# Kernel optimization log

Hardware: AMD Instinct MI355X
Metric: run time of the kernel (lower is better)

## Reference

```python
import jax, jax.numpy as jnp
import numpy as np

ALPHA = 300.0   # attractor_alpha
N_ATT = 16      # n_attractors
MIN_D = 0.001
MAX_D = 10.0


def _resize_bilinear_ac(x, out_h, out_w):
    """Bilinear resize with align_corners=True on trailing (H, W) dims of [B,C,h,w]."""
    h, w = x.shape[-2], x.shape[-1]
    ys = jnp.arange(out_h, dtype=jnp.float32) * ((h - 1) / max(out_h - 1, 1))
    xs = jnp.arange(out_w, dtype=jnp.float32) * ((w - 1) / max(out_w - 1, 1))
    y0 = jnp.floor(ys).astype(jnp.int32); y1 = jnp.minimum(y0 + 1, h - 1)
    x0 = jnp.floor(xs).astype(jnp.int32); x1 = jnp.minimum(x0 + 1, w - 1)
    wy = (ys - y0.astype(jnp.float32))[:, None]   # [out_h, 1]
    wx = (xs - x0.astype(jnp.float32))[None, :]   # [1, out_w]
    v00 = x[..., y0[:, None], x0[None, :]]
    v01 = x[..., y0[:, None], x1[None, :]]
    v10 = x[..., y1[:, None], x0[None, :]]
    v11 = x[..., y1[:, None], x1[None, :]]
    top = v00 * (1 - wx) + v01 * wx
    bot = v10 * (1 - wx) + v11 * wx
    return top * (1 - wy) + bot * wy


def setup_inputs() -> dict:
    key = jax.random.key(0)
    k = jax.random.split(key, 7)
    B, C, H, W = 4, 128, 192, 192
    n_bins = 64
    x = jax.random.normal(k[0], (B, C, H, W), dtype=jnp.float32)
    prev_bin = jax.random.uniform(k[1], (B, n_bins, H // 2, W // 2), dtype=jnp.float32)
    prev_bin_embedding = jax.random.normal(k[2], (B, C, H // 2, W // 2), dtype=jnp.float32)
    w1 = jax.random.normal(k[3], (128, 128), dtype=jnp.float32) * 0.05
    b1 = jnp.zeros((128,), dtype=jnp.float32)
    w2 = jax.random.normal(k[4], (2 * N_ATT, 128), dtype=jnp.float32) * 0.05
    b2 = jnp.zeros((2 * N_ATT,), dtype=jnp.float32)
    return {"x": x, "prev_bin": prev_bin, "prev_bin_embedding": prev_bin_embedding,
            "w1": w1, "b1": b1, "w2": w2, "b2": b2}


def reference(x, prev_bin, prev_bin_embedding, w1, b1, w2, b2):
    B, C, H, W = x.shape
    # add (interpolated) previous bin embedding
    pe = _resize_bilinear_ac(prev_bin_embedding, H, W)
    h = x + pe
    # per-pixel MLP (two 1x1 convs)
    h = jax.nn.relu(jnp.einsum('bchw,oc->bohw', h, w1) + b1[:, None, None])
    att = jax.nn.relu(jnp.einsum('bchw,oc->bohw', h, w2) + b2[:, None, None]) + 0.001
    # [B, n_attractors, 2, H, W] -> take normed attractor points
    att = att.reshape(B, N_ATT, 2, H, W)[:, :, 0]          # [B, nA, H, W]
    # upsample previous bin centers to feature resolution
    bc = _resize_bilinear_ac(prev_bin, H, W)               # [B, nB, H, W]
    # broadcast-subtract + inverse attractor + mean over attractors
    dx = att[:, :, None, :, :] - bc[:, None, :, :, :]      # [B, nA, nB, H, W]
    delta_c = jnp.mean(dx / (1.0 + ALPHA * dx * dx), axis=1)  # gamma = 2
    bin_new_centers = bc + delta_c
    bin_centers = (MAX_D - MIN_D) * bin_new_centers + MIN_D
    bin_centers = jnp.clip(jnp.sort(bin_centers, axis=1), MIN_D, MAX_D)
    return bin_new_centers, bin_centers
```

## Files before the change

kernel.cpp:

```cpp
#include <hip/hip_runtime.h>

constexpr int Bc = 4, Cc = 128, Hc = 192, Wc = 192;
constexpr int HI = 96, WI = 96;
constexpr int NB = 64;
constexpr int NA = 16;
constexpr float SCL = 95.0f / 191.0f;

typedef __attribute__((ext_vector_type(8))) short bf16x8;
typedef __attribute__((ext_vector_type(4))) float f32x4;

__device__ __forceinline__ unsigned short f2bf(float f) {
  unsigned u = __builtin_bit_cast(unsigned, f);
  unsigned r = (u + 0x7FFFu + ((u >> 16) & 1u)) >> 16;
  return (unsigned short)r;
}
__device__ __forceinline__ float rcp_fast(float r) {
#if defined(__has_builtin)
#if __has_builtin(__builtin_amdgcn_rcpf)
  return __builtin_amdgcn_rcpf(r);
#else
  return 1.0f / r;
#endif
#else
  return 1.0f / r;
#endif
}

__global__ __launch_bounds__(256) void k_prep(
    const float* __restrict__ w1, const float* __restrict__ w2,
    unsigned short* __restrict__ w1p, unsigned short* __restrict__ w2p)
{
  const int t = blockIdx.x * 256 + threadIdx.x;
  if (t < 16384) {
    const int e  = t & 7;
    const int l  = (t >> 3) & 63;
    const int kt = (t >> 9) & 3;
    const int nt = t >> 11;
    const int n  = nt * 16 + (l & 15);
    const int k  = kt * 32 + (l >> 4) * 8 + e;
    w1p[t] = f2bf(w1[n * 128 + k]);
  } else {
    const int u  = t - 16384;
    const int e  = u & 7;
    const int l  = (u >> 3) & 63;
    const int kt = u >> 9;
    const int n  = 2 * (l & 15);
    const int k  = kt * 32 + (l >> 4) * 8 + e;
    w2p[u] = f2bf(w2[n * 128 + k]);
  }
}

__global__ __launch_bounds__(256, 3) void k_att(
    const float* __restrict__ x, const float* __restrict__ pbe,
    const unsigned short* __restrict__ w1p, const float* __restrict__ b1,
    const unsigned short* __restrict__ w2p, const float* __restrict__ b2,
    float* __restrict__ att)
{
  constexpr int PH = 136;
  constexpr int RP = 37;
  __shared__ __align__(16) unsigned char smem[32768 + 128 * RP * 4];
  unsigned short* w1_s  = (unsigned short*)smem;
  float*          row_s = (float*)(smem + 32768);
  unsigned short* a1_s  = (unsigned short*)(smem + 32768);

  const int tid = threadIdx.x;
  const int xg0 = blockIdx.x * 64;
  const int y = blockIdx.y;
  const int b = blockIdx.z;

  const float ysf = y * SCL;
  const int y0 = (int)ysf;
  const int y1 = min(y0 + 1, HI - 1);
  const float wy = ysf - (float)y0;
  const int xi0 = (int)(xg0 * SCL);

  const int lane = tid & 63;
  const int wv = tid >> 6;
  const int ln = lane & 15;
  const int qd = lane >> 4;
  const int m0 = wv * 16;

  const int px = m0 + ln;
  const int xg = xg0 + px;
  const float xsf = (float)xg * SCL;
  const int x0i = (int)xsf;
  const float wx = xsf - (float)x0i;
  const int xl = x0i - xi0;

  float4 wstage[8];
  {
    const float4* wp4 = (const float4*)w1p;
    #pragma unroll
    for (int i = 0; i < 8; ++i) wstage[i] = wp4[tid + 256 * i];
  }

  bf16x8 b2f[4];
  #pragma unroll
  for (int kt = 0; kt < 4; ++kt)
    b2f[kt] = *(const bf16x8*)&w2p[kt * 512 + lane * 8];
  float bias1[8];
  #pragma unroll
  for (int nt = 0; nt < 8; ++nt) bias1[nt] = b1[nt * 16 + ln];
  const float bias2 = b2[2 * ln];

  float xr[32];
  #pragma unroll
  for (int kt = 0; kt < 4; ++kt) {
    #pragma unroll
    for (int j = 0; j < 8; ++j) {
      const int c = kt * 32 + qd * 8 + j;
      xr[kt * 8 + j] = x[((size_t)(b * Cc + c) * Hc + y) * Wc + xg];
    }
  }

  #pragma unroll
  for (int i = 0; i < 18; ++i) {
    const int f = tid + 256 * i;
    const int c = f / 36;
    const int xi = f - c * 36;
    const int xgl = min(xi0 + xi, WI - 1);
    const float* p = pbe + (size_t)(b * Cc + c) * (HI * WI);
    const float top = p[y0 * WI + xgl];
    const float bot = p[y1 * WI + xgl];
    row_s[c * RP + xi] = top + wy * (bot - top);
  }

  {
    float4* ws4 = (float4*)w1_s;
    #pragma unroll
    for (int i = 0; i < 8; ++i) ws4[tid + 256 * i] = wstage[i];
  }
  __syncthreads();

  bf16x8 af[4];
  #pragma unroll
  for (int kt = 0; kt < 4; ++kt) {
    #pragma unroll
    for (int j = 0; j < 8; ++j) {
      const int c = kt * 32 + qd * 8 + j;
      const float v0 = row_s[c * RP + xl];
      const float v1 = row_s[c * RP + xl + 1];
      af[kt][j] = (short)f2bf(xr[kt * 8 + j] + v0 + wx * (v1 - v0));
    }
  }
  __syncthreads();

  f32x4 acc[8];
  #pragma unroll
  for (int nt = 0; nt < 8; ++nt) acc[nt] = f32x4{0.f, 0.f, 0.f, 0.f};
  #pragma unroll
  for (int nt = 0; nt < 8; ++nt) {
    #pragma unroll
    for (int kt = 0; kt < 4; ++kt) {
      const bf16x8 bf = *(const bf16x8*)&w1_s[(nt * 4 + kt) * 512 + lane * 8];
      acc[nt] = __builtin_amdgcn_mfma_f32_16x16x32_bf16(af[kt], bf, acc[nt], 0, 0, 0);
    }
  }

  #pragma unroll
  for (int nt = 0; nt < 8; ++nt) {
    const int n = nt * 16 + ln;
    const float bias = bias1[nt];
    #pragma unroll
    for (int r = 0; r < 4; ++r) {
      const int m = m0 + qd * 4 + r;
      a1_s[m * PH + n] = f2bf(fmaxf(acc[nt][r] + bias, 0.f));
    }
  }

  f32x4 acc2 = f32x4{0.f, 0.f, 0.f, 0.f};
  #pragma unroll
  for (int kt = 0; kt < 4; ++kt) {
    const bf16x8 a2 = *(const bf16x8*)&a1_s[(m0 + ln) * PH + kt * 32 + qd * 8];
    acc2 = __builtin_amdgcn_mfma_f32_16x16x32_bf16(a2, b2f[kt], acc2, 0, 0, 0);
  }
  #pragma unroll
  for (int r = 0; r < 4; ++r) {
    const int opx = m0 + qd * 4 + r;
    const float v = fmaxf(acc2[r] + bias2, 0.f) + 0.001f;
    att[((size_t)((b * Hc + y) * Wc) + xg0 + opx) * NA + ln] = v;
  }
}

__global__ __launch_bounds__(192, 2) void k_bins(
    const float* __restrict__ pb, const float* __restrict__ att,
    float* __restrict__ out0, float* __restrict__ out1)
{
  __shared__ __align__(16) float row_s[NB][WI];

  const int tid = threadIdx.x;
  const int y = blockIdx.x;
  const int b = blockIdx.y;

  const float ysf = y * SCL;
  const int y0 = (int)ysf;
  const int y1 = min(y0 + 1, HI - 1);
  const float wy = ysf - (float)y0;

  float am[16];
  {
    const float4* ap = (const float4*)(att + ((size_t)((b * Hc + y) * Wc) + tid) * NA);
    const float4 a0 = ap[0], a1 = ap[1], a2 = ap[2], a3 = ap[3];
    am[0] = a0.x;  am[1] = a0.y;  am[2] = a0.z;  am[3] = a0.w;
    am[4] = a1.x;  am[5] = a1.y;  am[6] = a1.z;  am[7] = a1.w;
    am[8] = a2.x;  am[9] = a2.y;  am[10] = a2.z; am[11] = a2.w;
    am[12] = a3.x; am[13] = a3.y; am[14] = a3.z; am[15] = a3.w;
  }

  #pragma unroll
  for (int i = 0; i < 8; ++i) {
    const int u = tid + 192 * i;
    const int k = u / 24;
    const int g = u - k * 24;
    const float* base = pb + (size_t)(b * NB + k) * (HI * WI);
    const float4 t4 = *(const float4*)&base[y0 * WI + g * 4];
    const float4 b4 = *(const float4*)&base[y1 * WI + g * 4];
    float4 r;
    r.x = t4.x + wy * (b4.x - t4.x);
    r.y = t4.y + wy * (b4.y - t4.y);
    r.z = t4.z + wy * (b4.z - t4.z);
    r.w = t4.w + wy * (b4.w - t4.w);
    *(float4*)&row_s[k][g * 4] = r;
  }
  __syncthreads();

  const float xsf = tid * SCL;
  const int x0 = (int)xsf;
  const float wx = xsf - (float)x0;

  const size_t obase = (size_t)(b * NB) * (Hc * Wc) + (size_t)y * Wc + tid;
  float v[NB];

  #pragma unroll
  for (int kb = 0; kb < NB; kb += 4) {
    float bc[4], dl[4];
    #pragma unroll
    for (int q = 0; q < 4; ++q) {
      const int k = kb + q;
      const float v0 = row_s[k][x0], v1 = row_s[k][x0 + 1];
      bc[q] = v0 + wx * (v1 - v0);
      dl[q] = 0.f;
    }
    #pragma unroll
    for (int j = 0; j < NA; ++j) {
      const float a = am[j];
      #pragma unroll
      for (int q = 0; q < 4; ++q) {
        const float d = a - bc[q];
        const float rq = fmaf(300.f * d, d, 1.f);
        dl[q] = fmaf(d, rcp_fast(rq), dl[q]);
      }
    }
    #pragma unroll
    for (int q = 0; q < 4; ++q) {
      const float bnc = fmaf(dl[q], 1.f / 16.f, bc[q]);
      out0[obase + (size_t)(kb + q) * (Hc * Wc)] = bnc;
      v[kb + q] = fmaf(9.999f, bnc, 0.001f);
    }
  }

  #pragma unroll
  for (int size = 2; size <= NB; size <<= 1) {
    #pragma unroll
    for (int stride = size >> 1; stride >= 1; stride >>= 1) {
      #pragma unroll
      for (int i = 0; i < NB; ++i) {
        if ((i & stride) == 0) {
          const int j = i | stride;
          const bool asc = ((i & size) == 0);
          const float a = v[i], c = v[j];
          const float lo = fminf(a, c), hi = fmaxf(a, c);
          v[i] = asc ? lo : hi;
          v[j] = asc ? hi : lo;
        }
      }
    }
  }

  #pragma unroll
  for (int k = 0; k < NB; ++k) {
    out1[obase + (size_t)k * (Hc * Wc)] = fminf(fmaxf(v[k], 0.001f), 10.0f);
  }
}

extern "C" void kernel_launch(void* const* d_in, const int* in_sizes, int n_in,
                              void* d_out, int out_size, void* d_ws, size_t ws_size,
                              hipStream_t stream) {
  const float* x   = (const float*)d_in[0];
  const float* pb  = (const float*)d_in[1];
  const float* pbe = (const float*)d_in[2];
  const float* w1  = (const float*)d_in[3];
  const float* b1  = (const float*)d_in[4];
  const float* w2  = (const float*)d_in[5];
  const float* b2  = (const float*)d_in[6];

  float* out0 = (float*)d_out;
  float* out1 = out0 + (size_t)Bc * NB * Hc * Wc;

  unsigned short* w1p = (unsigned short*)d_ws;
  unsigned short* w2p = w1p + 16384;
  float* att = (float*)((char*)d_ws + 65536);

  k_prep<<<72, 256, 0, stream>>>(w1, w2, w1p, w2p);

  dim3 g1(Wc / 64, Hc, Bc);
  k_att<<<g1, 256, 0, stream>>>(x, pbe, w1p, b1, w2p, b2, att);

  dim3 g2(Hc, Bc);
  k_bins<<<g2, 192, 0, stream>>>(pb, att, out0, out1);
}
```

Baseline: 217.3 us.

## Split k_bins bins across two thread halves with shared-memory bitonic merge

Each pixel is now handled by two threads, each computing and sorting 32 of the 64 bins in opposite directions. The halves are then merged through shared memory with a compare-exchange step followed by a 32-element bitonic merge. This halves per-thread register use (v[32] instead of v[64]) and doubles block size so occupancy and parallelism rise. In exchange it adds extra syncthreads and shared-memory traffic, and each attractor load is duplicated across the two halves.

Result: faster. 213.0 us (-2.0%).

```diff
diff --git a/kernel.cpp b/kernel.cpp
--- a/kernel.cpp
+++ b/kernel.cpp
@@ -182,13 +182,16 @@
   }
 }
 
-__global__ __launch_bounds__(192, 2) void k_bins(
+__global__ __launch_bounds__(384, 4) void k_bins(
     const float* __restrict__ pb, const float* __restrict__ att,
     float* __restrict__ out0, float* __restrict__ out1)
 {
   __shared__ __align__(16) float row_s[NB][WI];
+  float* xch = &row_s[0][0];
 
   const int tid = threadIdx.x;
+  const int h = (tid >= 192) ? 1 : 0;
+  const int px = tid - 192 * h;
   const int y = blockIdx.x;
   const int b = blockIdx.y;
 
@@ -199,7 +202,7 @@
 
   float am[16];
   {
-    const float4* ap = (const float4*)(att + ((size_t)((b * Hc + y) * Wc) + tid) * NA);
+    const float4* ap = (const float4*)(att + ((size_t)((b * Hc + y) * Wc) + px) * NA);
     const float4 a0 = ap[0], a1 = ap[1], a2 = ap[2], a3 = ap[3];
     am[0] = a0.x;  am[1] = a0.y;  am[2] = a0.z;  am[3] = a0.w;
     am[4] = a1.x;  am[5] = a1.y;  am[6] = a1.z;  am[7] = a1.w;
@@ -208,8 +211,8 @@
   }
 
   #pragma unroll
-  for (int i = 0; i < 8; ++i) {
-    const int u = tid + 192 * i;
+  for (int i = 0; i < 4; ++i) {
+    const int u = tid + 384 * i;
     const int k = u / 24;
     const int g = u - k * 24;
     const float* base = pb + (size_t)(b * NB + k) * (HI * WI);
@@ -224,19 +227,19 @@
   }
   __syncthreads();
 
-  const float xsf = tid * SCL;
+  const float xsf = px * SCL;
   const int x0 = (int)xsf;
   const float wx = xsf - (float)x0;
 
-  const size_t obase = (size_t)(b * NB) * (Hc * Wc) + (size_t)y * Wc + tid;
-  float v[NB];
-
-  #pragma unroll
-  for (int kb = 0; kb < NB; kb += 4) {
+  const size_t obase = (size_t)(b * NB) * (Hc * Wc) + (size_t)y * Wc + px;
+  float v[32];
+
+  #pragma unroll
+  for (int kb = 0; kb < 32; kb += 4) {
     float bc[4], dl[4];
     #pragma unroll
     for (int q = 0; q < 4; ++q) {
-      const int k = kb + q;
+      const int k = h * 32 + kb + q;
       const float v0 = row_s[k][x0], v1 = row_s[k][x0 + 1];
       bc[q] = v0 + wx * (v1 - v0);
       dl[q] = 0.f;
@@ -254,32 +257,79 @@
     #pragma unroll
     for (int q = 0; q < 4; ++q) {
       const float bnc = fmaf(dl[q], 1.f / 16.f, bc[q]);
-      out0[obase + (size_t)(kb + q) * (Hc * Wc)] = bnc;
+      out0[obase + (size_t)(h * 32 + kb + q) * (Hc * Wc)] = bnc;
       v[kb + q] = fmaf(9.999f, bnc, 0.001f);
     }
   }
 
-  #pragma unroll
-  for (int size = 2; size <= NB; size <<= 1) {
-    #pragma unroll
-    for (int stride = size >> 1; stride >= 1; stride >>= 1) {
+  if (h == 0) {
+    #pragma unroll
+    for (int size = 2; size <= 32; size <<= 1)
       #pragma unroll
-      for (int i = 0; i < NB; ++i) {
-        if ((i & stride) == 0) {
-          const int j = i | stride;
-          const bool asc = ((i & size) == 0);
-          const float a = v[i], c = v[j];
-          const float lo = fminf(a, c), hi = fmaxf(a, c);
-          v[i] = asc ? lo : hi;
-          v[j] = asc ? hi : lo;
-        }
+      for (int stride = size >> 1; stride >= 1; stride >>= 1)
+        #pragma unroll
+        for (int i = 0; i < 32; ++i)
+          if ((i & stride) == 0) {
+            const int j = i | stride;
+            const bool asc = ((i & size) == 0);
+            const float a = v[i], c = v[j];
+            const float lo = fminf(a, c), hi = fmaxf(a, c);
+            v[i] = asc ? lo : hi;
+            v[j] = asc ? hi : lo;
+          }
+  } else {
+    #pragma unroll
+    for (int size = 2; size <= 32; size <<= 1)
+      #pragma unroll
+      for (int stride = size >> 1; stride >= 1; stride >>= 1)
+        #pragma unroll
+        for (int i = 0; i < 32; ++i)
+          if ((i & stride) == 0) {
+            const int j = i | stride;
+            const bool asc = ((i & size) != 0);
+            const float a = v[i], c = v[j];
+            const float lo = fminf(a, c), hi = fmaxf(a, c);
+            v[i] = asc ? lo : hi;
+            v[j] = asc ? hi : lo;
+          }
+  }
+
+  __syncthreads();
+  if (h) {
+    #pragma unroll
+    for (int i = 0; i < 32; ++i) xch[i * 192 + px] = v[i];
+  }
+  __syncthreads();
+  if (!h) {
+    #pragma unroll
+    for (int i = 0; i < 32; ++i) {
+      const float o = xch[i * 192 + px];
+      const float mn = fminf(v[i], o), mx = fmaxf(v[i], o);
+      v[i] = mn;
+      xch[i * 192 + px] = mx;
+    }
+  }
+  __syncthreads();
+  if (h) {
+    #pragma unroll
+    for (int i = 0; i < 32; ++i) v[i] = xch[i * 192 + px];
+  }
+
+  #pragma unroll
+  for (int stride = 16; stride >= 1; stride >>= 1)
+    #pragma unroll
+    for (int i = 0; i < 32; ++i)
+      if ((i & stride) == 0) {
+        const int j = i | stride;
+        const float a = v[i], c = v[j];
+        v[i] = fminf(a, c);
+        v[j] = fmaxf(a, c);
       }
-    }
-  }
-
-  #pragma unroll
-  for (int k = 0; k < NB; ++k) {
-    out1[obase + (size_t)k * (Hc * Wc)] = fminf(fmaxf(v[k], 0.001f), 10.0f);
+
+  #pragma unroll
+  for (int i = 0; i < 32; ++i) {
+    out1[obase + (size_t)(h * 32 + i) * (Hc * Wc)] =
+        fminf(fmaxf(v[i], 0.001f), 10.0f);
   }
 }
 
@@ -307,5 +357,5 @@
   k_att<<<g1, 256, 0, stream>>>(x, pbe, w1p, b1, w2p, b2, att);
 
   dim3 g2(Hc, Bc);
-  k_bins<<<g2, 192, 0, stream>>>(pb, att, out0, out1);
-}
+  k_bins<<<g2, 384, 0, stream>>>(pb, att, out0, out1);
+}
```
